# Performance work log

Hardware: AMD Instinct MI355X
Metric: run time of the kernel (lower is better)

## Reference

```python
import jax, jax.numpy as jnp
import numpy as np

B, C, N = 4, 192, 4096
K = 16                      # avg degree
E = B * N * K               # 262144 edges
C_OUT = 384


def setup_inputs() -> dict:
    key = jax.random.key(0)
    k1, k2, k3, k4 = jax.random.split(key, 4)
    x = jax.random.normal(k1, (B, C, N, 1), dtype=jnp.float32)
    edge_index = jax.random.randint(k2, (2, E), 0, B * N, dtype=jnp.int64)
    # BasicConv([2C, C_OUT]): 1x1 Conv2d + bias + ReLU (norm=None)
    W = jax.random.normal(k3, (C_OUT, 2 * C), dtype=jnp.float32) * (1.0 / np.sqrt(2 * C))
    b = jax.random.normal(k4, (C_OUT,), dtype=jnp.float32) * 0.01
    return {"x": x, "edge_index": edge_index, "W": W, "b": b}


def reference(x, edge_index, W, b):
    Bs, Cs, Ns, _ = x.shape
    BN = Bs * Ns
    # (B,C,N,1) -> flattened node table (B*N, C); node id = b*N + n
    x_flat = jnp.transpose(x[..., 0], (0, 2, 1)).reshape(BN, Cs)
    x_i = x_flat[edge_index[0]]          # (E, C) gather at dst
    x_j = x_flat[edge_index[1]]          # (E, C) gather at src
    diff = x_j - x_i
    # scatter-max over dst nodes; torch_scatter fills empty segments with 0
    agg = jax.ops.segment_max(diff, edge_index[0], num_segments=BN)
    agg = jnp.where(jnp.isfinite(agg), agg, 0.0)
    x_j_out = jnp.transpose(agg.reshape(Bs, Ns, Cs), (0, 2, 1))[..., None]  # (B,C,N,1)
    # interleave channels: cat along new axis 2 then reshape -> (B, 2C, N, 1)
    cat = jnp.stack([x, x_j_out], axis=2).reshape(Bs, 2 * Cs, Ns, 1)
    # 1x1 conv == GEMM over channels, + bias + ReLU
    out = jnp.einsum('oc,bcnw->bonw', W, cat) + b[None, :, None, None]
    return jax.nn.relu(out)
```

## Files before the change

### kernel.cpp

```cpp
#include <hip/hip_runtime.h>
#include <hip/hip_bf16.h>
#include <math.h>

#define Bz    4
#define Cch   192
#define Nn    4096
#define BN    16384
#define Ecnt  262144
#define COUT  384
#define CAP   64
#define MSTR  200

typedef __attribute__((ext_vector_type(8))) short short8;
typedef __attribute__((ext_vector_type(4))) float floatx4;

__device__ __forceinline__ float b2f(unsigned short u) {
    union { unsigned int i; float f; } z; z.i = ((unsigned int)u) << 16; return z.f;
}
__device__ __forceinline__ unsigned short f2b(float f) {
    __hip_bfloat16 h = __float2bfloat16(f);
    return *(unsigned short*)&h;
}

#define RED8(mm, FLD) do {                                                    \
    float a_ = fmaxf(fmaxf(b2f(v[0].FLD), b2f(v[1].FLD)),                     \
                     fmaxf(b2f(v[2].FLD), b2f(v[3].FLD)));                    \
    float b_ = fmaxf(fmaxf(b2f(v[4].FLD), b2f(v[5].FLD)),                     \
                     fmaxf(b2f(v[6].FLD), b2f(v[7].FLD)));                    \
    mm = fmaxf(mm, fmaxf(a_, b_)); } while (0)

__global__ __launch_bounds__(256) void prep_kernel(
    const float* __restrict__ x, const float* __restrict__ W,
    __hip_bfloat16* __restrict__ xb, __hip_bfloat16* __restrict__ Wxa,
    __hip_bfloat16* __restrict__ Wa, int* __restrict__ deg) {
    int bid = blockIdx.x;
    if (bid < 3072) {
        __shared__ float tile[32][33];
        int b = bid / 768;
        int r = bid - b * 768;
        int c0 = (r >> 7) * 32;
        int n0 = (r & 127) * 32;
        int tx = threadIdx.x & 31, ty = threadIdx.x >> 5;
        for (int i = ty; i < 32; i += 8)
            tile[i][tx] = x[((size_t)(b * Cch + c0 + i)) * Nn + n0 + tx];
        __syncthreads();
        for (int i = ty; i < 32; i += 8)
            xb[((size_t)(b * Nn + n0 + i)) * Cch + c0 + tx] =
                __float2bfloat16(tile[tx][i]);
    } else if (bid < 3360) {
        int i = (bid - 3072) * 256 + threadIdx.x;
        int o = i / Cch, c = i - o * Cch;
        float wx = W[o * 2 * Cch + 2 * c];
        float wa = W[o * 2 * Cch + 2 * c + 1];
        Wxa[i] = __float2bfloat16(wx - wa);
        Wa[i]  = __float2bfloat16(wa);
    } else {
        deg[(bid - 3360) * 256 + threadIdx.x] = 0;
    }
}

__device__ __forceinline__ void fill_body(
    int d0, int d1, int s0, int s1, int* deg, int* slots) {
    int p0 = atomicAdd(&deg[d0], 1); if (p0 < CAP) slots[(d0 << 6) + p0] = s0;
    int p1 = atomicAdd(&deg[d1], 1); if (p1 < CAP) slots[(d1 << 6) + p1] = s1;
}
__global__ __launch_bounds__(256) void fill64_kernel(
    const int* __restrict__ ew, int* __restrict__ deg, int* __restrict__ slots) {
    int t = blockIdx.x * 256 + threadIdx.x;
    int4 dv = *(const int4*)&ew[4 * t];
    int4 sv = *(const int4*)&ew[2 * Ecnt + 4 * t];
    fill_body(dv.x, dv.z, sv.x, sv.z, deg, slots);
}
__global__ __launch_bounds__(256) void fill32_kernel(
    const int* __restrict__ ew, int* __restrict__ deg, int* __restrict__ slots) {
    int t = blockIdx.x * 256 + threadIdx.x;
    int2 dv = *(const int2*)&ew[2 * t];
    int2 sv = *(const int2*)&ew[Ecnt + 2 * t];
    fill_body(dv.x, dv.y, sv.x, sv.y, deg, slots);
}

#define MFMA3()                                                                \
    acc0 = __builtin_amdgcn_mfma_f32_16x16x32_bf16(b0, af0, acc0, 0, 0, 0);    \
    acc1 = __builtin_amdgcn_mfma_f32_16x16x32_bf16(b1, af0, acc1, 0, 0, 0);    \
    acc2 = __builtin_amdgcn_mfma_f32_16x16x32_bf16(b2, af0, acc2, 0, 0, 0)

__global__ __launch_bounds__(512, 4) void p2_kernel(
    const int* __restrict__ deg, const int* __restrict__ slots,
    const __hip_bfloat16* __restrict__ xb,
    const __hip_bfloat16* __restrict__ Wxa, const __hip_bfloat16* __restrict__ Wa,
    const float* __restrict__ bias, float* __restrict__ out)
{
    __shared__ __align__(16) unsigned short Xs[16 * MSTR];
    __shared__ __align__(16) unsigned short Ms[16 * MSTR];
    int tid = threadIdx.x, bid = blockIdx.x;
    int lane = tid & 63, wave = tid >> 6;
    int quad = lane >> 4, lrow = lane & 15;
    int node0 = bid * 16;
    const unsigned short* xbu = (const unsigned short*)xb;
    int act = lane < 48;
    int cb = lane * 4;

    int dd[2], nbr[2];
#pragma unroll
    for (int q = 0; q < 2; q++) {
        int node = node0 + wave * 2 + q;
        int d = deg[node]; if (d > CAP) d = CAP;
        dd[q] = __builtin_amdgcn_readfirstlane(d);
        nbr[q] = (lane < dd[q]) ? slots[(node << 6) + lane] : 0;
    }
#pragma unroll
    for (int q = 0; q < 2; q++) {
        int nl = wave * 2 + q;
        int node = node0 + nl;
        int d = dd[q], nbrval = nbr[q];
        ushort4 xv = {0, 0, 0, 0};
        if (act) xv = *(const ushort4*)&xbu[node * Cch + cb];
        float m0 = -INFINITY, m1 = -INFINITY, m2 = -INFINITY, m3 = -INFINITY;
        int k = 0;
        for (; k + 8 <= d; k += 8) {
            int s[8];
#pragma unroll
            for (int u = 0; u < 8; u++) s[u] = __builtin_amdgcn_readlane(nbrval, k + u);
            if (act) {
                ushort4 v[8];
#pragma unroll
                for (int u = 0; u < 8; u++) v[u] = *(const ushort4*)&xbu[s[u] * Cch + cb];
                RED8(m0, x); RED8(m1, y); RED8(m2, z); RED8(m3, w);
            }
        }
        if (k + 4 <= d) {
            int s0 = __builtin_amdgcn_readlane(nbrval, k);
            int s1 = __builtin_amdgcn_readlane(nbrval, k + 1);
            int s2 = __builtin_amdgcn_readlane(nbrval, k + 2);
            int s3 = __builtin_amdgcn_readlane(nbrval, k + 3);
            if (act) {
                ushort4 v0 = *(const ushort4*)&xbu[s0 * Cch + cb];
                ushort4 v1 = *(const ushort4*)&xbu[s1 * Cch + cb];
                ushort4 v2 = *(const ushort4*)&xbu[s2 * Cch + cb];
                ushort4 v3 = *(const ushort4*)&xbu[s3 * Cch + cb];
                m0 = fmaxf(m0, fmaxf(fmaxf(b2f(v0.x), b2f(v1.x)), fmaxf(b2f(v2.x), b2f(v3.x))));
                m1 = fmaxf(m1, fmaxf(fmaxf(b2f(v0.y), b2f(v1.y)), fmaxf(b2f(v2.y), b2f(v3.y))));
                m2 = fmaxf(m2, fmaxf(fmaxf(b2f(v0.z), b2f(v1.z)), fmaxf(b2f(v2.z), b2f(v3.z))));
                m3 = fmaxf(m3, fmaxf(fmaxf(b2f(v0.w), b2f(v1.w)), fmaxf(b2f(v2.w), b2f(v3.w))));
            }
            k += 4;
        }
        for (; k < d; k++) {
            int s = __builtin_amdgcn_readlane(nbrval, k);
            if (act) {
                ushort4 v = *(const ushort4*)&xbu[s * Cch + cb];
                m0 = fmaxf(m0, b2f(v.x)); m1 = fmaxf(m1, b2f(v.y));
                m2 = fmaxf(m2, b2f(v.z)); m3 = fmaxf(m3, b2f(v.w));
            }
        }
        if (act) {
            *(ushort4*)&Xs[nl * MSTR + cb] = xv;
            ushort4 o4;
            if (d > 0) {
                o4.x = f2b(m0); o4.y = f2b(m1); o4.z = f2b(m2); o4.w = f2b(m3);
            } else {
                o4 = xv;
            }
            *(ushort4*)&Ms[nl * MSTR + cb] = o4;
        }
    }
    __syncthreads();

    floatx4 acc0 = {}, acc1 = {}, acc2 = {};
    const unsigned short* Wx16 = (const unsigned short*)Wxa;
    const unsigned short* Wa16 = (const unsigned short*)Wa;
    size_t w0 = (size_t)(wave * 48 +  0 + lrow) * Cch;
    size_t w1 = (size_t)(wave * 48 + 16 + lrow) * Cch;
    size_t w2 = (size_t)(wave * 48 + 32 + lrow) * Cch;
    int kq = quad * 8;

    short8 b0 = *(const short8*)&Wx16[w0 + kq];
    short8 b1 = *(const short8*)&Wx16[w1 + kq];
    short8 b2 = *(const short8*)&Wx16[w2 + kq];
#pragma unroll
    for (int s = 0; s < 12; s++) {
        short8 n0, n1, n2;
        if (s < 11) {
            int sn = s + 1;
            const unsigned short* Wn = (sn >= 6) ? Wa16 : Wx16;
            int kkn = ((sn >= 6) ? sn - 6 : sn) * 32 + kq;
            n0 = *(const short8*)&Wn[w0 + kkn];
            n1 = *(const short8*)&Wn[w1 + kkn];
            n2 = *(const short8*)&Wn[w2 + kkn];
        }
        int kk = ((s >= 6) ? s - 6 : s) * 32 + kq;
        const unsigned short* Ar = (s >= 6) ? Ms : Xs;
        short8 af0 = *(const short8*)&Ar[lrow * MSTR + kk];
        MFMA3();
        if (s < 11) { b0 = n0; b1 = n1; b2 = n2; }
    }

    floatx4 accs[3] = {acc0, acc1, acc2};
    int node = node0 + lrow;
    int b = node >> 12, n = node & 4095;
#pragma unroll
    for (int j = 0; j < 3; j++) {
        int ob = wave * 48 + j * 16 + quad * 4;
#pragma unroll
        for (int r = 0; r < 4; r++) {
            int o = ob + r;
            float v = accs[j][r] + bias[o];
            out[((size_t)(b * COUT + o)) * Nn + n] = fmaxf(v, 0.0f);
        }
    }
}

extern "C" void kernel_launch(void* const* d_in, const int* in_sizes, int n_in,
                              void* d_out, int out_size, void* d_ws, size_t ws_size,
                              hipStream_t stream) {
    const float* x    = (const float*)d_in[0];
    const int*   ew   = (const int*)d_in[1];
    const float* W    = (const float*)d_in[2];
    const float* bias = (const float*)d_in[3];
    float* out        = (float*)d_out;

    char* ws = (char*)d_ws;
    __hip_bfloat16* xb   = (__hip_bfloat16*)ws;
    __hip_bfloat16* Wxa  = (__hip_bfloat16*)(ws + 12582912);
    __hip_bfloat16* Wa   = (__hip_bfloat16*)(ws + 12730368);
    int* deg   = (int*)(ws + 12877824);
    int* slots = (int*)(ws + 12943360);

    bool is64 = (in_sizes[1] >= (int)(2u * Ecnt * 8u));

    prep_kernel<<<3424, 256, 0, stream>>>(x, W, xb, Wxa, Wa, deg);
    if (is64)
        fill64_kernel<<<Ecnt / 512, 256, 0, stream>>>(ew, deg, slots);
    else
        fill32_kernel<<<Ecnt / 512, 256, 0, stream>>>(ew, deg, slots);
    p2_kernel<<<BN / 16, 512, 0, stream>>>(deg, slots, xb, Wxa, Wa, bias, out);
}
```

Baseline: 135.2 us.

## Process 32 nodes per block, hoist neighbor loads, add 16-wide gather unroll

Doubles the node tile per block from 16 to 32 so each wave loads its weight fragments once and reuses them across two MFMA row tiles, halving global weight traffic per node. Degree, slot and self-feature loads for all four nodes of a wave are issued up front to overlap their latency. The neighbor max-gather also gains a 16-way unrolled path for more memory-level parallelism. The costs are more registers per thread, double the LDS, and half as many blocks, which may reduce occupancy and load balance.

```diff
diff --git a/kernel.cpp b/kernel.cpp
--- a/kernel.cpp
+++ b/kernel.cpp
@@ -27,6 +27,17 @@
                      fmaxf(b2f(v[2].FLD), b2f(v[3].FLD)));                    \
     float b_ = fmaxf(fmaxf(b2f(v[4].FLD), b2f(v[5].FLD)),                     \
                      fmaxf(b2f(v[6].FLD), b2f(v[7].FLD)));                    \
+    mm = fmaxf(mm, fmaxf(a_, b_)); } while (0)
+
+#define RED16(mm, FLD) do {                                                   \
+    float a_ = fmaxf(fmaxf(fmaxf(b2f(v[0].FLD), b2f(v[1].FLD)),               \
+                           fmaxf(b2f(v[2].FLD), b2f(v[3].FLD))),              \
+                     fmaxf(fmaxf(b2f(v[4].FLD), b2f(v[5].FLD)),               \
+                           fmaxf(b2f(v[6].FLD), b2f(v[7].FLD))));             \
+    float b_ = fmaxf(fmaxf(fmaxf(b2f(v[8].FLD), b2f(v[9].FLD)),               \
+                           fmaxf(b2f(v[10].FLD), b2f(v[11].FLD))),            \
+                     fmaxf(fmaxf(b2f(v[12].FLD), b2f(v[13].FLD)),             \
+                           fmaxf(b2f(v[14].FLD), b2f(v[15].FLD))));           \
     mm = fmaxf(mm, fmaxf(a_, b_)); } while (0)
 
 __global__ __launch_bounds__(256) void prep_kernel(
@@ -79,10 +90,13 @@
     fill_body(dv.x, dv.y, sv.x, sv.y, deg, slots);
 }
 
-#define MFMA3()                                                                \
-    acc0 = __builtin_amdgcn_mfma_f32_16x16x32_bf16(b0, af0, acc0, 0, 0, 0);    \
-    acc1 = __builtin_amdgcn_mfma_f32_16x16x32_bf16(b1, af0, acc1, 0, 0, 0);    \
-    acc2 = __builtin_amdgcn_mfma_f32_16x16x32_bf16(b2, af0, acc2, 0, 0, 0)
+#define MFMA6()                                                                \
+    acc00 = __builtin_amdgcn_mfma_f32_16x16x32_bf16(b0, af0, acc00, 0, 0, 0);  \
+    acc10 = __builtin_amdgcn_mfma_f32_16x16x32_bf16(b0, af1, acc10, 0, 0, 0);  \
+    acc01 = __builtin_amdgcn_mfma_f32_16x16x32_bf16(b1, af0, acc01, 0, 0, 0);  \
+    acc11 = __builtin_amdgcn_mfma_f32_16x16x32_bf16(b1, af1, acc11, 0, 0, 0);  \
+    acc02 = __builtin_amdgcn_mfma_f32_16x16x32_bf16(b2, af0, acc02, 0, 0, 0);  \
+    acc12 = __builtin_amdgcn_mfma_f32_16x16x32_bf16(b2, af1, acc12, 0, 0, 0)
 
 __global__ __launch_bounds__(512, 4) void p2_kernel(
     const int* __restrict__ deg, const int* __restrict__ slots,
@@ -90,33 +104,46 @@
     const __hip_bfloat16* __restrict__ Wxa, const __hip_bfloat16* __restrict__ Wa,
     const float* __restrict__ bias, float* __restrict__ out)
 {
-    __shared__ __align__(16) unsigned short Xs[16 * MSTR];
-    __shared__ __align__(16) unsigned short Ms[16 * MSTR];
+    __shared__ __align__(16) unsigned short Xs[32 * MSTR];
+    __shared__ __align__(16) unsigned short Ms[32 * MSTR];
     int tid = threadIdx.x, bid = blockIdx.x;
     int lane = tid & 63, wave = tid >> 6;
     int quad = lane >> 4, lrow = lane & 15;
-    int node0 = bid * 16;
+    int node0 = bid * 32;
     const unsigned short* xbu = (const unsigned short*)xb;
     int act = lane < 48;
     int cb = lane * 4;
 
-    int dd[2], nbr[2];
-#pragma unroll
-    for (int q = 0; q < 2; q++) {
-        int node = node0 + wave * 2 + q;
-        int d = deg[node]; if (d > CAP) d = CAP;
-        dd[q] = __builtin_amdgcn_readfirstlane(d);
-        nbr[q] = (lane < dd[q]) ? slots[(node << 6) + lane] : 0;
-    }
-#pragma unroll
-    for (int q = 0; q < 2; q++) {
-        int nl = wave * 2 + q;
-        int node = node0 + nl;
-        int d = dd[q], nbrval = nbr[q];
-        ushort4 xv = {0, 0, 0, 0};
-        if (act) xv = *(const ushort4*)&xbu[node * Cch + cb];
+    int dd[4], nbrv[4];
+    ushort4 xv[4];
+#pragma unroll
+    for (int q = 0; q < 4; q++) {
+        int node = node0 + wave * 4 + q;
+        dd[q]   = deg[node];
+        nbrv[q] = slots[(node << 6) + lane];
+        xv[q]   = act ? *(const ushort4*)&xbu[node * Cch + cb]
+                      : (ushort4){0, 0, 0, 0};
+    }
+
+#pragma unroll
+    for (int q = 0; q < 4; q++) {
+        int nl = wave * 4 + q;
+        int d = dd[q]; if (d > CAP) d = CAP;
+        d = __builtin_amdgcn_readfirstlane(d);
+        int nbrval = nbrv[q];
         float m0 = -INFINITY, m1 = -INFINITY, m2 = -INFINITY, m3 = -INFINITY;
         int k = 0;
+        for (; k + 16 <= d; k += 16) {
+            int s[16];
+#pragma unroll
+            for (int u = 0; u < 16; u++) s[u] = __builtin_amdgcn_readlane(nbrval, k + u);
+            if (act) {
+                ushort4 v[16];
+#pragma unroll
+                for (int u = 0; u < 16; u++) v[u] = *(const ushort4*)&xbu[s[u] * Cch + cb];
+                RED16(m0, x); RED16(m1, y); RED16(m2, z); RED16(m3, w);
+            }
+        }
         for (; k + 8 <= d; k += 8) {
             int s[8];
 #pragma unroll
@@ -154,19 +181,19 @@
             }
         }
         if (act) {
-            *(ushort4*)&Xs[nl * MSTR + cb] = xv;
+            *(ushort4*)&Xs[nl * MSTR + cb] = xv[q];
             ushort4 o4;
             if (d > 0) {
                 o4.x = f2b(m0); o4.y = f2b(m1); o4.z = f2b(m2); o4.w = f2b(m3);
             } else {
-                o4 = xv;
+                o4 = xv[q];
             }
             *(ushort4*)&Ms[nl * MSTR + cb] = o4;
         }
     }
     __syncthreads();
 
-    floatx4 acc0 = {}, acc1 = {}, acc2 = {};
+    floatx4 acc00 = {}, acc01 = {}, acc02 = {}, acc10 = {}, acc11 = {}, acc12 = {};
     const unsigned short* Wx16 = (const unsigned short*)Wxa;
     const unsigned short* Wa16 = (const unsigned short*)Wa;
     size_t w0 = (size_t)(wave * 48 +  0 + lrow) * Cch;
@@ -191,21 +218,25 @@
         int kk = ((s >= 6) ? s - 6 : s) * 32 + kq;
         const unsigned short* Ar = (s >= 6) ? Ms : Xs;
         short8 af0 = *(const short8*)&Ar[lrow * MSTR + kk];
-        MFMA3();
+        short8 af1 = *(const short8*)&Ar[(16 + lrow) * MSTR + kk];
+        MFMA6();
         if (s < 11) { b0 = n0; b1 = n1; b2 = n2; }
     }
 
-    floatx4 accs[3] = {acc0, acc1, acc2};
-    int node = node0 + lrow;
-    int b = node >> 12, n = node & 4095;
-#pragma unroll
-    for (int j = 0; j < 3; j++) {
-        int ob = wave * 48 + j * 16 + quad * 4;
-#pragma unroll
-        for (int r = 0; r < 4; r++) {
-            int o = ob + r;
-            float v = accs[j][r] + bias[o];
-            out[((size_t)(b * COUT + o)) * Nn + n] = fmaxf(v, 0.0f);
+    floatx4 accs[2][3] = {{acc00, acc01, acc02}, {acc10, acc11, acc12}};
+#pragma unroll
+    for (int i = 0; i < 2; i++) {
+        int node = node0 + i * 16 + lrow;
+        int b = node >> 12, n = node & 4095;
+#pragma unroll
+        for (int j = 0; j < 3; j++) {
+            int ob = wave * 48 + j * 16 + quad * 4;
+#pragma unroll
+            for (int r = 0; r < 4; r++) {
+                int o = ob + r;
+                float v = accs[i][j][r] + bias[o];
+                out[((size_t)(b * COUT + o)) * Nn + n] = fmaxf(v, 0.0f);
+            }
         }
     }
 }
@@ -233,5 +264,5 @@
         fill64_kernel<<<Ecnt / 512, 256, 0, stream>>>(ew, deg, slots);
     else
         fill32_kernel<<<Ecnt / 512, 256, 0, stream>>>(ew, deg, slots);
-    p2_kernel<<<BN / 16, 512, 0, stream>>>(deg, slots, xb, Wxa, Wa, bias, out);
-}
+    p2_kernel<<<BN / 32, 512, 0, stream>>>(deg, slots, xb, Wxa, Wa, bias, out);
+}
```

Measured after the change: 120.7 us. 10.7% less time.
